# Optimization experiments

Measured on AMD Instinct MI355X. Metric: run time of the kernel, lower is better.

## Reference

```python
import jax, jax.numpy as jnp
import numpy as np


def setup_inputs() -> dict:
    B, I, H = 4096, 512, 1024
    key = jax.random.key(0)
    ks = jax.random.split(key, 10)
    return {
        "input": jax.random.normal(ks[0], (B, I), dtype=jnp.float32),
        "t": jax.random.uniform(ks[1], (B, 1), dtype=jnp.float32),
        "hx": jax.random.normal(ks[2], (B, H), dtype=jnp.float32),
        "cx": jax.random.normal(ks[3], (B, H), dtype=jnp.float32),
        "weight_ih": jax.random.normal(ks[4], (4 * H, I), dtype=jnp.float32),
        "weight_hh": jax.random.normal(ks[5], (4 * H, H), dtype=jnp.float32),
        "bias_ih": jax.random.normal(ks[6], (4 * H,), dtype=jnp.float32),
        "bias_hh": jax.random.normal(ks[7], (4 * H,), dtype=jnp.float32),
        "W_decomp": jax.random.normal(ks[8], (H, H), dtype=jnp.float32),
        "b_decomp": jax.random.normal(ks[9], (H,), dtype=jnp.float32),
    }


def reference(input, t, hx, cx, weight_ih, weight_hh, bias_ih, bias_hh, W_decomp, b_decomp):
    H = W_decomp.shape[0]
    # gates: [B, 4H]
    gates = input @ weight_ih.T + bias_ih + hx @ weight_hh.T + bias_hh
    ingate, forgetgate, cellgate, outgate = jnp.split(gates, 4, axis=1)
    # time-decay factor g(t): elementwise 1/t where t != 0, broadcast [B,1] -> [B,H]
    T = jnp.where(t != 0, 1.0 / jnp.where(t != 0, t, 1.0), 0.0)  # [B, 1]
    T = jnp.broadcast_to(T, (t.shape[0], H))
    # T-LSTM cell-state decomposition
    C_ST = jnp.tanh(cx @ W_decomp + b_decomp)
    cx_adj = cx - C_ST + T * C_ST
    ingate = jax.nn.sigmoid(ingate)
    forgetgate = jax.nn.sigmoid(forgetgate)
    cellgate = jnp.tanh(cellgate)
    outgate = jax.nn.sigmoid(outgate)
    cy = forgetgate * cx_adj + ingate * cellgate
    hy = outgate * jnp.tanh(cy)
    return (hy, cy)
```

## Files before the change

kernel.cpp:

```cpp
#include <hip/hip_runtime.h>
#include <cstdint>


typedef __attribute__((ext_vector_type(8))) __bf16 bf16x8;
typedef __attribute__((ext_vector_type(4))) float f32x4;

__device__ __forceinline__ unsigned short f2bf_rn(float f) {
  unsigned int u = __float_as_uint(f);
  unsigned int r = u + 0x7fffu + ((u >> 16) & 1u);
  return (unsigned short)(r >> 16);
}
__device__ __forceinline__ float bf2f(unsigned short h) {
  return __uint_as_float(((unsigned int)h) << 16);
}
__device__ __forceinline__ float sigm_f(float x) {
  return 1.0f / (1.0f + __expf(-x));
}
__device__ __forceinline__ float tanh_f(float x) {
  return 1.0f - 2.0f / (__expf(2.0f * x) + 1.0f);
}
__device__ __forceinline__ void gl_lds16(const void* g, void* l) {
  __builtin_amdgcn_global_load_lds(
      (const __attribute__((address_space(1))) void*)g,
      (__attribute__((address_space(3))) void*)l, 16, 0, 0);
}

__global__ __launch_bounds__(384) void prep_k(
    const float* __restrict__ input, const float* __restrict__ hx,
    const float* __restrict__ w_ih, const float* __restrict__ w_hh,
    const float* __restrict__ cx,
    unsigned short* __restrict__ Xhi, unsigned short* __restrict__ Xlo,
    unsigned short* __restrict__ Whi, unsigned short* __restrict__ Wlo,
    unsigned short* __restrict__ Chi, unsigned short* __restrict__ Clo) {
  const int bid = blockIdx.x;
  const int k = threadIdx.x << 2;
  const float* src;
  unsigned short *hi, *lo;
  if (bid < 4096) {
    const long m = bid;
    src = (k < 512) ? (input + m * 512 + k) : (hx + m * 1024 + (k - 512));
    hi = Xhi + m * 1536 + k;
    lo = Xlo + m * 1536 + k;
  } else if (bid < 8192) {
    const int n = bid - 4096;
    const int g = n >> 10;
    const int h = n & 1023;
    const long nd = ((h >> 5) << 7) | (g << 5) | (h & 31);
    src = (k < 512) ? (w_ih + (long)n * 512 + k) : (w_hh + (long)n * 1024 + (k - 512));
    hi = Whi + nd * 1536 + k;
    lo = Wlo + nd * 1536 + k;
  } else {
    if (k >= 1024) return;
    const long m = bid - 8192;
    src = cx + m * 1024 + k;
    hi = Chi + m * 1024 + k;
    lo = Clo + m * 1024 + k;
  }
  float4 v = *(const float4*)src;
  ushort4 hv, lv;
  hv.x = f2bf_rn(v.x); lv.x = f2bf_rn(v.x - bf2f(hv.x));
  hv.y = f2bf_rn(v.y); lv.y = f2bf_rn(v.y - bf2f(hv.y));
  hv.z = f2bf_rn(v.z); lv.z = f2bf_rn(v.z - bf2f(hv.z));
  hv.w = f2bf_rn(v.w); lv.w = f2bf_rn(v.w - bf2f(hv.w));
  *(ushort4*)hi = hv;
  *(ushort4*)lo = lv;
}

__global__ void transpose_split_k(const float* __restrict__ W, int Ndim,
                                  unsigned short* __restrict__ Thi,
                                  unsigned short* __restrict__ Tlo) {
  __shared__ float tile[64][65];
  const int bx = blockIdx.x * 64;
  const int by = blockIdx.y * 64;
  const int tx = threadIdx.x;
  for (int r = threadIdx.y; r < 64; r += 4)
    tile[r][tx] = W[(long)(by + r) * Ndim + bx + tx];
  __syncthreads();
  for (int r = threadIdx.y; r < 64; r += 4) {
    float v = tile[tx][r];
    unsigned short h = f2bf_rn(v);
    long o = (long)(bx + r) * Ndim + by + tx;
    Thi[o] = h;
    Tlo[o] = f2bf_rn(v - bf2f(h));
  }
}

__global__ __launch_bounds__(256) void gemm_mega(
    const unsigned short* __restrict__ Xh, const unsigned short* __restrict__ Xl,
    const unsigned short* __restrict__ Wh, const unsigned short* __restrict__ Wl,
    const unsigned short* __restrict__ Ch, const unsigned short* __restrict__ Cl,
    const unsigned short* __restrict__ Dh, const unsigned short* __restrict__ Dl,
    const float* __restrict__ b_ih, const float* __restrict__ b_hh,
    const float* __restrict__ b_d, const float* __restrict__ cx,
    const float* __restrict__ t, float* __restrict__ out) {
  __shared__ __align__(16) unsigned short sAh[128 * 32];
  __shared__ __align__(16) unsigned short sAl[128 * 32];
  __shared__ __align__(16) unsigned short sBh[128 * 32];
  __shared__ __align__(16) unsigned short sBl[128 * 32];

  const int n_blk = blockIdx.x & 31;
  const int m_blk = blockIdx.x >> 5;
  const int m0 = m_blk * 128;
  const int n0 = n_blk * 128;
  const int h0 = n_blk * 32;

  const int tid = threadIdx.x;
  const int wave = tid >> 6;
  const int lane = tid & 63;
  const int srow = lane >> 2;
  const int ssw = (((lane & 3) ^ ((lane >> 3) & 3)) << 3);
  const int fm = lane & 15;
  const int fq = lane >> 4;
  const int psw = (fq ^ ((fm >> 1) & 3)) << 3;

  f32x4 dacc[2][2];
#pragma unroll
  for (int i = 0; i < 2; ++i)
#pragma unroll
    for (int j = 0; j < 2; ++j) dacc[i][j] = {0.f, 0.f, 0.f, 0.f};

  {
    const unsigned short* dsrc = (wave < 2) ? Dh : Dl;
    unsigned short* ddst = ((wave < 2) ? sBh : sBl) + ((wave & 1) * 16) * 32;
    const long dgbase = (long)(h0 + (wave & 1) * 16 + srow) * 1024 + ssw;
    for (int kt = 0; kt < 1024; kt += 32) {
#pragma unroll
      for (int r = 0; r < 2; ++r) {
        const int rowb = r * 64 + wave * 16;
        const long gA = (long)(m0 + rowb + srow) * 1024 + kt + ssw;
        gl_lds16(Ch + gA, sAh + rowb * 32);
        gl_lds16(Cl + gA, sAl + rowb * 32);
      }
      gl_lds16(dsrc + dgbase + kt, ddst);
      __syncthreads();
      bf16x8 ah[2], al[2], bh[2], bl[2];
#pragma unroll
      for (int i = 0; i < 2; ++i) {
        const int ao = (wave * 32 + i * 16 + fm) * 32 + psw;
        ah[i] = *(const bf16x8*)(sAh + ao);
        al[i] = *(const bf16x8*)(sAl + ao);
        const int bo = (i * 16 + fm) * 32 + psw;
        bh[i] = *(const bf16x8*)(sBh + bo);
        bl[i] = *(const bf16x8*)(sBl + bo);
      }
#pragma unroll
      for (int i = 0; i < 2; ++i)
#pragma unroll
        for (int j = 0; j < 2; ++j) {
          dacc[i][j] = __builtin_amdgcn_mfma_f32_16x16x32_bf16(ah[i], bh[j], dacc[i][j], 0, 0, 0);
          dacc[i][j] = __builtin_amdgcn_mfma_f32_16x16x32_bf16(ah[i], bl[j], dacc[i][j], 0, 0, 0);
          dacc[i][j] = __builtin_amdgcn_mfma_f32_16x16x32_bf16(al[i], bh[j], dacc[i][j], 0, 0, 0);
        }
      __syncthreads();
    }
  }

  f32x4 acc[2][8];
#pragma unroll
  for (int i = 0; i < 2; ++i)
#pragma unroll
    for (int j = 0; j < 8; ++j) acc[i][j] = {0.f, 0.f, 0.f, 0.f};

  for (int kt = 0; kt < 1536; kt += 32) {
#pragma unroll
    for (int r = 0; r < 2; ++r) {
      const int rowb = r * 64 + wave * 16;
      const long gA = (long)(m0 + rowb + srow) * 1536 + kt + ssw;
      const long gB = (long)(n0 + rowb + srow) * 1536 + kt + ssw;
      gl_lds16(Xh + gA, sAh + rowb * 32);
      gl_lds16(Xl + gA, sAl + rowb * 32);
      gl_lds16(Wh + gB, sBh + rowb * 32);
      gl_lds16(Wl + gB, sBl + rowb * 32);
    }
    __syncthreads();
    bf16x8 ah[2], al[2];
#pragma unroll
    for (int i = 0; i < 2; ++i) {
      const int ao = (wave * 32 + i * 16 + fm) * 32 + psw;
      ah[i] = *(const bf16x8*)(sAh + ao);
      al[i] = *(const bf16x8*)(sAl + ao);
    }
#pragma unroll
    for (int jh = 0; jh < 2; ++jh) {
      bf16x8 bh[4], bl[4];
#pragma unroll
      for (int jj = 0; jj < 4; ++jj) {
        const int bo = ((jh * 4 + jj) * 16 + fm) * 32 + psw;
        bh[jj] = *(const bf16x8*)(sBh + bo);
        bl[jj] = *(const bf16x8*)(sBl + bo);
      }
#pragma unroll
      for (int i = 0; i < 2; ++i)
#pragma unroll
        for (int jj = 0; jj < 4; ++jj) {
          const int j = jh * 4 + jj;
          acc[i][j] = __builtin_amdgcn_mfma_f32_16x16x32_bf16(ah[i], bh[jj], acc[i][j], 0, 0, 0);
          acc[i][j] = __builtin_amdgcn_mfma_f32_16x16x32_bf16(ah[i], bl[jj], acc[i][j], 0, 0, 0);
          acc[i][j] = __builtin_amdgcn_mfma_f32_16x16x32_bf16(al[i], bh[jj], acc[i][j], 0, 0, 0);
        }
    }
    __syncthreads();
  }

#pragma unroll
  for (int j0 = 0; j0 < 2; ++j0) {
    const int h = h0 + j0 * 16 + fm;
    const float bsum_i = b_ih[h]           + b_hh[h];
    const float bsum_f = b_ih[1024 + h]    + b_hh[1024 + h];
    const float bsum_g = b_ih[2048 + h]    + b_hh[2048 + h];
    const float bsum_o = b_ih[3072 + h]    + b_hh[3072 + h];
    const float bd = b_d[h];
#pragma unroll
    for (int i = 0; i < 2; ++i) {
#pragma unroll
      for (int r = 0; r < 4; ++r) {
        const int m = m0 + wave * 32 + i * 16 + fq * 4 + r;
        const float tv = t[m];
        const float T = (tv != 0.0f) ? (1.0f / tv) : 0.0f;
        const float cst = tanh_f(dacc[i][j0][r] + bd);
        const float cadj = cx[(long)m * 1024 + h] + (T - 1.0f) * cst;
        const float ig = sigm_f(acc[i][0 + j0][r] + bsum_i);
        const float fg = sigm_f(acc[i][2 + j0][r] + bsum_f);
        const float cg = tanh_f(acc[i][4 + j0][r] + bsum_g);
        const float og = sigm_f(acc[i][6 + j0][r] + bsum_o);
        const float cy = fg * cadj + ig * cg;
        const float hy = og * tanh_f(cy);
        out[(long)m * 1024 + h] = hy;
        out[4096L * 1024 + (long)m * 1024 + h] = cy;
      }
    }
  }
}

extern "C" void kernel_launch(void* const* d_in, const int* in_sizes, int n_in,
                              void* d_out, int out_size, void* d_ws, size_t ws_size,
                              hipStream_t stream) {
  const float* input = (const float*)d_in[0];
  const float* t     = (const float*)d_in[1];
  const float* hx    = (const float*)d_in[2];
  const float* cx    = (const float*)d_in[3];
  const float* w_ih  = (const float*)d_in[4];
  const float* w_hh  = (const float*)d_in[5];
  const float* b_ih  = (const float*)d_in[6];
  const float* b_hh  = (const float*)d_in[7];
  const float* Wd    = (const float*)d_in[8];
  const float* b_d   = (const float*)d_in[9];

  const long B = 4096, H = 1024, KX = 1536, NG = 4096;

  char* ws = (char*)d_ws;
  unsigned short* Xhi = (unsigned short*)ws; ws += B * KX * 2;
  unsigned short* Xlo = (unsigned short*)ws; ws += B * KX * 2;
  unsigned short* Whi = (unsigned short*)ws; ws += NG * KX * 2;
  unsigned short* Wlo = (unsigned short*)ws; ws += NG * KX * 2;
  unsigned short* Chi = (unsigned short*)ws; ws += B * H * 2;
  unsigned short* Clo = (unsigned short*)ws; ws += B * H * 2;
  unsigned short* Dhi = (unsigned short*)ws; ws += H * H * 2;
  unsigned short* Dlo = (unsigned short*)ws; ws += H * H * 2;

  prep_k<<<12288, 384, 0, stream>>>(input, hx, w_ih, w_hh, cx,
                                    Xhi, Xlo, Whi, Wlo, Chi, Clo);
  transpose_split_k<<<dim3(16, 16), dim3(64, 4), 0, stream>>>(Wd, 1024, Dhi, Dlo);
  gemm_mega<<<1024, 256, 0, stream>>>(Xhi, Xlo, Whi, Wlo, Chi, Clo, Dhi, Dlo,
                                      b_ih, b_hh, b_d, cx, t, (float*)d_out);
}
```

Before: 329.8 us.

## Switch GEMM to 32x32x16 MFMA with direct-register A loads and merge prep kernels

The main GEMM now uses 32x32x16 bf16 MFMA tiles and a K step of 64. A operands are loaded straight from global memory into registers, and only B goes through a swizzled LDS buffer, so A no longer needs LDS staging. The two prep kernels, the split conversion and the Wd transpose, are merged into one launch with 16-element-per-thread vectorized conversion. Together these aim to cut LDS traffic, barrier count per K element and launch overhead. The cost is uncoalesced per-lane global A loads with no reuse across waves, plus higher register pressure.

```diff
diff --git a/kernel.cpp b/kernel.cpp
--- a/kernel.cpp
+++ b/kernel.cpp
@@ -3,7 +3,8 @@
 
 
 typedef __attribute__((ext_vector_type(8))) __bf16 bf16x8;
-typedef __attribute__((ext_vector_type(4))) float f32x4;
+typedef __attribute__((ext_vector_type(16))) float f32x16;
+typedef __attribute__((ext_vector_type(8))) unsigned short ushort8;
 
 __device__ __forceinline__ unsigned short f2bf_rn(float f) {
   unsigned int u = __float_as_uint(f);
@@ -25,63 +26,76 @@
       (__attribute__((address_space(3))) void*)l, 16, 0, 0);
 }
 
-__global__ __launch_bounds__(384) void prep_k(
+__device__ __forceinline__ void cvt16(const float* __restrict__ s,
+                                      unsigned short* __restrict__ hi,
+                                      unsigned short* __restrict__ lo) {
+  float4 v[4];
+#pragma unroll
+  for (int i = 0; i < 4; ++i) v[i] = ((const float4*)s)[i];
+  const float* f = (const float*)v;
+  ushort8 h[2], l[2];
+#pragma unroll
+  for (int i = 0; i < 16; ++i) {
+    unsigned short hh = f2bf_rn(f[i]);
+    ((unsigned short*)h)[i] = hh;
+    ((unsigned short*)l)[i] = f2bf_rn(f[i] - bf2f(hh));
+  }
+  ((ushort8*)hi)[0] = h[0];
+  ((ushort8*)hi)[1] = h[1];
+  ((ushort8*)lo)[0] = l[0];
+  ((ushort8*)lo)[1] = l[1];
+}
+
+__global__ __launch_bounds__(256) void prep_k(
     const float* __restrict__ input, const float* __restrict__ hx,
     const float* __restrict__ w_ih, const float* __restrict__ w_hh,
-    const float* __restrict__ cx,
+    const float* __restrict__ cx, const float* __restrict__ Wd,
     unsigned short* __restrict__ Xhi, unsigned short* __restrict__ Xlo,
     unsigned short* __restrict__ Whi, unsigned short* __restrict__ Wlo,
-    unsigned short* __restrict__ Chi, unsigned short* __restrict__ Clo) {
+    unsigned short* __restrict__ Chi, unsigned short* __restrict__ Clo,
+    unsigned short* __restrict__ Dhi, unsigned short* __restrict__ Dlo) {
   const int bid = blockIdx.x;
-  const int k = threadIdx.x << 2;
-  const float* src;
-  unsigned short *hi, *lo;
-  if (bid < 4096) {
-    const long m = bid;
-    src = (k < 512) ? (input + m * 512 + k) : (hx + m * 1024 + (k - 512));
-    hi = Xhi + m * 1536 + k;
-    lo = Xlo + m * 1536 + k;
-  } else if (bid < 8192) {
-    const int n = bid - 4096;
+  const int tid = threadIdx.x;
+  if (bid < 1536) {
+    const int u = bid * 256 + tid;
+    const int row = u / 96;
+    const int col = (u % 96) << 4;
+    const float* src = (col < 512) ? (input + (long)row * 512 + col)
+                                   : (hx + (long)row * 1024 + (col - 512));
+    cvt16(src, Xhi + (long)row * 1536 + col, Xlo + (long)row * 1536 + col);
+  } else if (bid < 3072) {
+    const int u = (bid - 1536) * 256 + tid;
+    const int n = u / 96;
+    const int col = (u % 96) << 4;
     const int g = n >> 10;
     const int h = n & 1023;
     const long nd = ((h >> 5) << 7) | (g << 5) | (h & 31);
-    src = (k < 512) ? (w_ih + (long)n * 512 + k) : (w_hh + (long)n * 1024 + (k - 512));
-    hi = Whi + nd * 1536 + k;
-    lo = Wlo + nd * 1536 + k;
+    const float* src = (col < 512) ? (w_ih + (long)n * 512 + col)
+                                   : (w_hh + (long)n * 1024 + (col - 512));
+    cvt16(src, Whi + nd * 1536 + col, Wlo + nd * 1536 + col);
+  } else if (bid < 4096) {
+    const int u = (bid - 3072) * 256 + tid;
+    const int row = u >> 6;
+    const int col = (u & 63) << 4;
+    cvt16(cx + (long)row * 1024 + col, Chi + (long)row * 1024 + col,
+          Clo + (long)row * 1024 + col);
   } else {
-    if (k >= 1024) return;
-    const long m = bid - 8192;
-    src = cx + m * 1024 + k;
-    hi = Chi + m * 1024 + k;
-    lo = Clo + m * 1024 + k;
-  }
-  float4 v = *(const float4*)src;
-  ushort4 hv, lv;
-  hv.x = f2bf_rn(v.x); lv.x = f2bf_rn(v.x - bf2f(hv.x));
-  hv.y = f2bf_rn(v.y); lv.y = f2bf_rn(v.y - bf2f(hv.y));
-  hv.z = f2bf_rn(v.z); lv.z = f2bf_rn(v.z - bf2f(hv.z));
-  hv.w = f2bf_rn(v.w); lv.w = f2bf_rn(v.w - bf2f(hv.w));
-  *(ushort4*)hi = hv;
-  *(ushort4*)lo = lv;
-}
-
-__global__ void transpose_split_k(const float* __restrict__ W, int Ndim,
-                                  unsigned short* __restrict__ Thi,
-                                  unsigned short* __restrict__ Tlo) {
-  __shared__ float tile[64][65];
-  const int bx = blockIdx.x * 64;
-  const int by = blockIdx.y * 64;
-  const int tx = threadIdx.x;
-  for (int r = threadIdx.y; r < 64; r += 4)
-    tile[r][tx] = W[(long)(by + r) * Ndim + bx + tx];
-  __syncthreads();
-  for (int r = threadIdx.y; r < 64; r += 4) {
-    float v = tile[tx][r];
-    unsigned short h = f2bf_rn(v);
-    long o = (long)(bx + r) * Ndim + by + tx;
-    Thi[o] = h;
-    Tlo[o] = f2bf_rn(v - bf2f(h));
+    __shared__ float tile[64][65];
+    const int bid2 = bid - 4096;
+    const int bx = (bid2 & 15) * 64;
+    const int by = (bid2 >> 4) * 64;
+    const int tx = tid & 63;
+    const int ty = tid >> 6;
+    for (int r = ty; r < 64; r += 4)
+      tile[r][tx] = Wd[(long)(by + r) * 1024 + bx + tx];
+    __syncthreads();
+    for (int r = ty; r < 64; r += 4) {
+      float v = tile[tx][r];
+      unsigned short h = f2bf_rn(v);
+      long o = (long)(bx + r) * 1024 + by + tx;
+      Dhi[o] = h;
+      Dlo[o] = f2bf_rn(v - bf2f(h));
+    }
   }
 }
 
@@ -93,10 +107,8 @@
     const float* __restrict__ b_ih, const float* __restrict__ b_hh,
     const float* __restrict__ b_d, const float* __restrict__ cx,
     const float* __restrict__ t, float* __restrict__ out) {
-  __shared__ __align__(16) unsigned short sAh[128 * 32];
-  __shared__ __align__(16) unsigned short sAl[128 * 32];
-  __shared__ __align__(16) unsigned short sBh[128 * 32];
-  __shared__ __align__(16) unsigned short sBl[128 * 32];
+  __shared__ __align__(16) unsigned short sBh[128 * 64];
+  __shared__ __align__(16) unsigned short sBl[128 * 64];
 
   const int n_blk = blockIdx.x & 31;
   const int m_blk = blockIdx.x >> 5;
@@ -107,128 +119,107 @@
   const int tid = threadIdx.x;
   const int wave = tid >> 6;
   const int lane = tid & 63;
-  const int srow = lane >> 2;
-  const int ssw = (((lane & 3) ^ ((lane >> 3) & 3)) << 3);
-  const int fm = lane & 15;
-  const int fq = lane >> 4;
-  const int psw = (fq ^ ((fm >> 1) & 3)) << 3;
-
-  f32x4 dacc[2][2];
-#pragma unroll
-  for (int i = 0; i < 2; ++i)
-#pragma unroll
-    for (int j = 0; j < 2; ++j) dacc[i][j] = {0.f, 0.f, 0.f, 0.f};
-
+  const int lm = lane & 31;
+  const int lk = lane >> 5;
+  const int lmw = lm & 7;
+  const int sg = lane >> 3;
+  const int sq = (lane & 7) ^ sg;
+
+  f32x16 dacc;
+#pragma unroll
+  for (int r = 0; r < 16; ++r) dacc[r] = 0.f;
   {
-    const unsigned short* dsrc = (wave < 2) ? Dh : Dl;
-    unsigned short* ddst = ((wave < 2) ? sBh : sBl) + ((wave & 1) * 16) * 32;
-    const long dgbase = (long)(h0 + (wave & 1) * 16 + srow) * 1024 + ssw;
-    for (int kt = 0; kt < 1024; kt += 32) {
-#pragma unroll
-      for (int r = 0; r < 2; ++r) {
-        const int rowb = r * 64 + wave * 16;
-        const long gA = (long)(m0 + rowb + srow) * 1024 + kt + ssw;
-        gl_lds16(Ch + gA, sAh + rowb * 32);
-        gl_lds16(Cl + gA, sAl + rowb * 32);
-      }
-      gl_lds16(dsrc + dgbase + kt, ddst);
-      __syncthreads();
-      bf16x8 ah[2], al[2], bh[2], bl[2];
-#pragma unroll
-      for (int i = 0; i < 2; ++i) {
-        const int ao = (wave * 32 + i * 16 + fm) * 32 + psw;
-        ah[i] = *(const bf16x8*)(sAh + ao);
-        al[i] = *(const bf16x8*)(sAl + ao);
-        const int bo = (i * 16 + fm) * 32 + psw;
-        bh[i] = *(const bf16x8*)(sBh + bo);
-        bl[i] = *(const bf16x8*)(sBl + bo);
-      }
-#pragma unroll
-      for (int i = 0; i < 2; ++i)
-#pragma unroll
-        for (int j = 0; j < 2; ++j) {
-          dacc[i][j] = __builtin_amdgcn_mfma_f32_16x16x32_bf16(ah[i], bh[j], dacc[i][j], 0, 0, 0);
-          dacc[i][j] = __builtin_amdgcn_mfma_f32_16x16x32_bf16(ah[i], bl[j], dacc[i][j], 0, 0, 0);
-          dacc[i][j] = __builtin_amdgcn_mfma_f32_16x16x32_bf16(al[i], bh[j], dacc[i][j], 0, 0, 0);
+    const long arow = (long)(m0 + wave * 32 + lm) * 1024 + lk * 8;
+    const long brow = (long)(h0 + wave * 8 + sg) * 1024 + sq * 8;
+    unsigned short* dsth = sBh + (wave * 8) * 64;
+    unsigned short* dstl = sBl + (wave * 8) * 64;
+    for (int kt = 0; kt < 1024; kt += 64) {
+      bf16x8 ah[4], al[4];
+#pragma unroll
+      for (int kh = 0; kh < 4; ++kh) {
+        ah[kh] = *(const bf16x8*)(Ch + arow + kt + kh * 16);
+        al[kh] = *(const bf16x8*)(Cl + arow + kt + kh * 16);
+      }
+      gl_lds16(Dh + brow + kt, dsth);
+      gl_lds16(Dl + brow + kt, dstl);
+      __syncthreads();
+#pragma unroll
+      for (int kh = 0; kh < 4; ++kh) {
+        const int pc = ((kh * 2 + lk) ^ lmw) << 3;
+        bf16x8 bh = *(const bf16x8*)(sBh + lm * 64 + pc);
+        bf16x8 bl = *(const bf16x8*)(sBl + lm * 64 + pc);
+        dacc = __builtin_amdgcn_mfma_f32_32x32x16_bf16(ah[kh], bh, dacc, 0, 0, 0);
+        dacc = __builtin_amdgcn_mfma_f32_32x32x16_bf16(ah[kh], bl, dacc, 0, 0, 0);
+        dacc = __builtin_amdgcn_mfma_f32_32x32x16_bf16(al[kh], bh, dacc, 0, 0, 0);
+      }
+      __syncthreads();
+    }
+  }
+
+  f32x16 acc[4];
+#pragma unroll
+  for (int j = 0; j < 4; ++j)
+#pragma unroll
+    for (int r = 0; r < 16; ++r) acc[j][r] = 0.f;
+  {
+    const long arow = (long)(m0 + wave * 32 + lm) * 1536 + lk * 8;
+    const long brow = (long)(n0 + wave * 32 + sg) * 1536 + sq * 8;
+    for (int kt = 0; kt < 1536; kt += 64) {
+      bf16x8 ah[4], al[4];
+#pragma unroll
+      for (int kh = 0; kh < 4; ++kh) {
+        ah[kh] = *(const bf16x8*)(Xh + arow + kt + kh * 16);
+        al[kh] = *(const bf16x8*)(Xl + arow + kt + kh * 16);
+      }
+#pragma unroll
+      for (int i = 0; i < 4; ++i) {
+        const long gb = brow + (long)i * 8 * 1536 + kt;
+        const int loff = (wave * 32 + i * 8) * 64;
+        gl_lds16(Wh + gb, sBh + loff);
+        gl_lds16(Wl + gb, sBl + loff);
+      }
+      __syncthreads();
+#pragma unroll
+      for (int kh = 0; kh < 4; ++kh) {
+        const int pc = ((kh * 2 + lk) ^ lmw) << 3;
+        bf16x8 bh[4], bl[4];
+#pragma unroll
+        for (int nb = 0; nb < 4; ++nb) {
+          bh[nb] = *(const bf16x8*)(sBh + (nb * 32 + lm) * 64 + pc);
+          bl[nb] = *(const bf16x8*)(sBl + (nb * 32 + lm) * 64 + pc);
         }
+#pragma unroll
+        for (int nb = 0; nb < 4; ++nb) {
+          acc[nb] = __builtin_amdgcn_mfma_f32_32x32x16_bf16(ah[kh], bh[nb], acc[nb], 0, 0, 0);
+          acc[nb] = __builtin_amdgcn_mfma_f32_32x32x16_bf16(ah[kh], bl[nb], acc[nb], 0, 0, 0);
+          acc[nb] = __builtin_amdgcn_mfma_f32_32x32x16_bf16(al[kh], bh[nb], acc[nb], 0, 0, 0);
+        }
+      }
       __syncthreads();
     }
   }
 
-  f32x4 acc[2][8];
-#pragma unroll
-  for (int i = 0; i < 2; ++i)
-#pragma unroll
-    for (int j = 0; j < 8; ++j) acc[i][j] = {0.f, 0.f, 0.f, 0.f};
-
-  for (int kt = 0; kt < 1536; kt += 32) {
-#pragma unroll
-    for (int r = 0; r < 2; ++r) {
-      const int rowb = r * 64 + wave * 16;
-      const long gA = (long)(m0 + rowb + srow) * 1536 + kt + ssw;
-      const long gB = (long)(n0 + rowb + srow) * 1536 + kt + ssw;
-      gl_lds16(Xh + gA, sAh + rowb * 32);
-      gl_lds16(Xl + gA, sAl + rowb * 32);
-      gl_lds16(Wh + gB, sBh + rowb * 32);
-      gl_lds16(Wl + gB, sBl + rowb * 32);
-    }
-    __syncthreads();
-    bf16x8 ah[2], al[2];
-#pragma unroll
-    for (int i = 0; i < 2; ++i) {
-      const int ao = (wave * 32 + i * 16 + fm) * 32 + psw;
-      ah[i] = *(const bf16x8*)(sAh + ao);
-      al[i] = *(const bf16x8*)(sAl + ao);
-    }
-#pragma unroll
-    for (int jh = 0; jh < 2; ++jh) {
-      bf16x8 bh[4], bl[4];
-#pragma unroll
-      for (int jj = 0; jj < 4; ++jj) {
-        const int bo = ((jh * 4 + jj) * 16 + fm) * 32 + psw;
-        bh[jj] = *(const bf16x8*)(sBh + bo);
-        bl[jj] = *(const bf16x8*)(sBl + bo);
-      }
-#pragma unroll
-      for (int i = 0; i < 2; ++i)
-#pragma unroll
-        for (int jj = 0; jj < 4; ++jj) {
-          const int j = jh * 4 + jj;
-          acc[i][j] = __builtin_amdgcn_mfma_f32_16x16x32_bf16(ah[i], bh[jj], acc[i][j], 0, 0, 0);
-          acc[i][j] = __builtin_amdgcn_mfma_f32_16x16x32_bf16(ah[i], bl[jj], acc[i][j], 0, 0, 0);
-          acc[i][j] = __builtin_amdgcn_mfma_f32_16x16x32_bf16(al[i], bh[jj], acc[i][j], 0, 0, 0);
-        }
-    }
-    __syncthreads();
-  }
-
-#pragma unroll
-  for (int j0 = 0; j0 < 2; ++j0) {
-    const int h = h0 + j0 * 16 + fm;
-    const float bsum_i = b_ih[h]           + b_hh[h];
-    const float bsum_f = b_ih[1024 + h]    + b_hh[1024 + h];
-    const float bsum_g = b_ih[2048 + h]    + b_hh[2048 + h];
-    const float bsum_o = b_ih[3072 + h]    + b_hh[3072 + h];
-    const float bd = b_d[h];
-#pragma unroll
-    for (int i = 0; i < 2; ++i) {
-#pragma unroll
-      for (int r = 0; r < 4; ++r) {
-        const int m = m0 + wave * 32 + i * 16 + fq * 4 + r;
-        const float tv = t[m];
-        const float T = (tv != 0.0f) ? (1.0f / tv) : 0.0f;
-        const float cst = tanh_f(dacc[i][j0][r] + bd);
-        const float cadj = cx[(long)m * 1024 + h] + (T - 1.0f) * cst;
-        const float ig = sigm_f(acc[i][0 + j0][r] + bsum_i);
-        const float fg = sigm_f(acc[i][2 + j0][r] + bsum_f);
-        const float cg = tanh_f(acc[i][4 + j0][r] + bsum_g);
-        const float og = sigm_f(acc[i][6 + j0][r] + bsum_o);
-        const float cy = fg * cadj + ig * cg;
-        const float hy = og * tanh_f(cy);
-        out[(long)m * 1024 + h] = hy;
-        out[4096L * 1024 + (long)m * 1024 + h] = cy;
-      }
-    }
+  const int h = h0 + lm;
+  const float bsum_i = b_ih[h] + b_hh[h];
+  const float bsum_f = b_ih[1024 + h] + b_hh[1024 + h];
+  const float bsum_g = b_ih[2048 + h] + b_hh[2048 + h];
+  const float bsum_o = b_ih[3072 + h] + b_hh[3072 + h];
+  const float bd = b_d[h];
+#pragma unroll
+  for (int reg = 0; reg < 16; ++reg) {
+    const int m = m0 + wave * 32 + (reg & 3) + 8 * (reg >> 2) + 4 * lk;
+    const float tv = t[m];
+    const float T = (tv != 0.0f) ? (1.0f / tv) : 0.0f;
+    const float cst = tanh_f(dacc[reg] + bd);
+    const float cadj = cx[(long)m * 1024 + h] + (T - 1.0f) * cst;
+    const float ig = sigm_f(acc[0][reg] + bsum_i);
+    const float fg = sigm_f(acc[1][reg] + bsum_f);
+    const float cg = tanh_f(acc[2][reg] + bsum_g);
+    const float og = sigm_f(acc[3][reg] + bsum_o);
+    const float cy = fg * cadj + ig * cg;
+    const float hy = og * tanh_f(cy);
+    out[(long)m * 1024 + h] = hy;
+    out[4096L * 1024 + (long)m * 1024 + h] = cy;
   }
 }
 
@@ -258,9 +249,8 @@
   unsigned short* Dhi = (unsigned short*)ws; ws += H * H * 2;
   unsigned short* Dlo = (unsigned short*)ws; ws += H * H * 2;
 
-  prep_k<<<12288, 384, 0, stream>>>(input, hx, w_ih, w_hh, cx,
-                                    Xhi, Xlo, Whi, Wlo, Chi, Clo);
-  transpose_split_k<<<dim3(16, 16), dim3(64, 4), 0, stream>>>(Wd, 1024, Dhi, Dlo);
+  prep_k<<<4352, 256, 0, stream>>>(input, hx, w_ih, w_hh, cx, Wd,
+                                   Xhi, Xlo, Whi, Wlo, Chi, Clo, Dhi, Dlo);
   gemm_mega<<<1024, 256, 0, stream>>>(Xhi, Xlo, Whi, Wlo, Chi, Clo, Dhi, Dlo,
                                       b_ih, b_hh, b_d, cx, t, (float*)d_out);
 }
```

Result: slower. 361.3 us (+9.5%).
